# Optimization experiments

Measured on AMD Instinct MI355X. Metric: run time of the kernel, lower is better.

Reference implementation:

```python
import jax, jax.numpy as jnp
import numpy as np

K = 7          # kernel_size (square)
P = K // 2     # padding
NUM_HEADS = 12


def setup_inputs() -> dict:
    key = jax.random.key(0)
    ks = jax.random.split(key, 6)
    B, H, W, D = 16, 56, 56, 768
    x = jax.random.normal(ks[0], (B, H, W, D), jnp.float32)
    qkv_w = jax.random.normal(ks[1], (3 * D, D), jnp.float32) * 0.02
    qkv_b = jnp.zeros((3 * D,), jnp.float32)
    rel_bias = jax.random.normal(ks[2], (1, NUM_HEADS, 1, K * K), jnp.float32)
    proj_w = jax.random.normal(ks[3], (D, D), jnp.float32) * 0.02
    proj_b = jnp.zeros((D,), jnp.float32)
    return {"x": x, "qkv_w": qkv_w, "qkv_b": qkv_b, "rel_bias": rel_bias,
            "proj_w": proj_w, "proj_b": proj_b}


def reference(x, qkv_w, qkv_b, rel_bias, proj_w, proj_b):
    B, H, W, D = x.shape
    hd = D // NUM_HEADS
    scale = 1.0 / np.sqrt(hd)

    qkv = x @ qkv_w.T + qkv_b                       # [B,H,W,3D]
    qkv = jnp.pad(qkv, ((0, 0), (P, P), (P, P), (0, 0)))  # zero-pad spatially
    Hp, Wp = H + 2 * P, W + 2 * P
    qkv = qkv.reshape(B, Hp, Wp, 3, NUM_HEADS, hd)
    qkv = jnp.transpose(qkv, (3, 0, 4, 1, 2, 5))    # [3,B,nh,Hp,Wp,hd]
    qf, kf, vf = qkv[0], qkv[1], qkv[2]

    q = qf[:, :, P:P + H, P:P + W, :]               # [B,nh,H,W,hd] (center pixel queries)

    # validity of each padded position (out-of-bounds keys get -inf, matching the torch mask)
    valid = jnp.pad(jnp.ones((H, W), dtype=bool), ((P, P), (P, P)))

    # scores per kernel offset; offsets iterate row-major (di, dj) matching
    # torch.meshgrid(..., indexing='ij') flattening used for relative_position_bias
    scores = []
    for di in range(K):
        for dj in range(K):
            ksh = kf[:, :, di:di + H, dj:dj + W, :]           # shifted keys [B,nh,H,W,hd]
            s = jnp.einsum('bnhwd,bnhwd->bnhw', q, ksh) * scale
            s = s + rel_bias[0, :, 0, di * K + dj][None, :, None, None]
            vmask = valid[di:di + H, dj:dj + W]
            s = jnp.where(vmask[None, None, :, :], s, -jnp.inf)
            scores.append(s)
    scores = jnp.stack(scores, axis=-1)             # [B,nh,H,W,K*K]
    attn = jax.nn.softmax(scores, axis=-1)

    out = jnp.zeros_like(q)
    for di in range(K):
        for dj in range(K):
            vsh = vf[:, :, di:di + H, dj:dj + W, :]
            out = out + attn[..., di * K + dj, None] * vsh

    out = jnp.transpose(out, (0, 2, 3, 1, 4)).reshape(B, H, W, D)
    return out @ proj_w.T + proj_b
```

## Files before the change

kernel.cpp:

```cpp
#include <hip/hip_runtime.h>
#include <hip/hip_bf16.h>

typedef __attribute__((ext_vector_type(8))) short short8;
typedef __attribute__((ext_vector_type(4))) short s16x4;
typedef __attribute__((ext_vector_type(4))) float f32x4;

#define AS1 __attribute__((address_space(1)))
#define AS3 __attribute__((address_space(3)))

__device__ __forceinline__ void gld16(const short* g, short* l) {
  __builtin_amdgcn_global_load_lds((const AS1 void*)g, (AS3 void*)l, 16, 0, 0);
}

__device__ __forceinline__ float bf2f(short x) {
  return __uint_as_float(((unsigned)(unsigned short)x) << 16);
}
__device__ __forceinline__ short f2bf(float f) {
  unsigned u = __float_as_uint(f);
  return (short)((u + 0x7fffu + ((u >> 16) & 1u)) >> 16);
}

__global__ void cast_f32_bf16(const float* __restrict__ src, short* __restrict__ dst, int n8) {
  int stride = gridDim.x * blockDim.x;
  for (int i = blockIdx.x * blockDim.x + threadIdx.x; i < n8; i += stride) {
    const float4* s = (const float4*)(src + (size_t)i * 8);
    float4 a = s[0], b = s[1];
    short8 o;
    o[0] = f2bf(a.x); o[1] = f2bf(a.y); o[2] = f2bf(a.z); o[3] = f2bf(a.w);
    o[4] = f2bf(b.x); o[5] = f2bf(b.y); o[6] = f2bf(b.z); o[7] = f2bf(b.w);
    *(short8*)(dst + (size_t)i * 8) = o;
  }
}

template<int OUT_BF16>
__global__ __launch_bounds__(256, 2) void gemm_bt(
    const short* __restrict__ A, const short* __restrict__ Bm,
    const float* __restrict__ bias, void* __restrict__ C,
    int M, int N, int Kd, int NB)
{
  __shared__ short As[128 * 64];
  __shared__ short Bs[128 * 64];
  const int tid = threadIdx.x;
  const int wave = tid >> 6, lane = tid & 63;

  int nwg = gridDim.x;
  int chunk = nwg >> 3;
  int bid = blockIdx.x;
  int nb2 = (bid & 7) * chunk + (bid >> 3);
  int per = NB << 3;
  int sr = nb2 / per, rem = nb2 - sr * per;
  int nblk = rem >> 3, mrow = rem & 7;
  int mblk = sr * 8 + mrow;

  size_t arow0 = (size_t)mblk * 128;
  size_t brow0 = (size_t)nblk * 128;
  const int wm = wave >> 1, wn = wave & 1;
  const int lr = lane & 15, grp = lane >> 4;

  const short* gsa[4]; const short* gsb[4];
  short* lda[4]; short* ldb[4];
  #pragma unroll
  for (int i = 0; i < 4; ++i) {
    int f = i * 256 + wave * 64 + lane;
    int row = f >> 3;
    int colc = (f & 7) ^ (row & 7);
    gsa[i] = A  + (arow0 + row) * Kd + colc * 8;
    gsb[i] = Bm + (brow0 + row) * Kd + colc * 8;
    lda[i] = &As[(i * 256 + wave * 64) * 8];
    ldb[i] = &Bs[(i * 256 + wave * 64) * 8];
  }

  f32x4 acc[4][4];
  #pragma unroll
  for (int i = 0; i < 4; ++i)
    #pragma unroll
    for (int j = 0; j < 4; ++j) {
      acc[i][j][0] = 0.f; acc[i][j][1] = 0.f; acc[i][j][2] = 0.f; acc[i][j][3] = 0.f;
    }

  int aoff[4][2], boff[4][2];
  #pragma unroll
  for (int mi = 0; mi < 4; ++mi) {
    int arow = wm * 64 + mi * 16 + lr;
    int brow = wn * 64 + mi * 16 + lr;
    #pragma unroll
    for (int kk = 0; kk < 2; ++kk) {
      int cb = (kk * 64 + grp * 16);
      aoff[mi][kk] = arow * 64 + ((cb ^ ((arow & 7) << 4)) >> 1);
      boff[mi][kk] = brow * 64 + ((cb ^ ((brow & 7) << 4)) >> 1);
    }
  }

  for (int k0 = 0; k0 < Kd; k0 += 64) {
    #pragma unroll
    for (int i = 0; i < 4; ++i) {
      gld16(gsa[i] + k0, lda[i]);
      gld16(gsb[i] + k0, ldb[i]);
    }
    __syncthreads();
    short8 af[4][2], bfr[4][2];
    #pragma unroll
    for (int mi = 0; mi < 4; ++mi)
      #pragma unroll
      for (int kk = 0; kk < 2; ++kk) {
        af[mi][kk]  = *(const short8*)&As[aoff[mi][kk]];
        bfr[mi][kk] = *(const short8*)&Bs[boff[mi][kk]];
      }
    #pragma unroll
    for (int kk = 0; kk < 2; ++kk)
      #pragma unroll
      for (int i = 0; i < 4; ++i)
        #pragma unroll
        for (int j = 0; j < 4; ++j)
          acc[i][j] = __builtin_amdgcn_mfma_f32_16x16x32_bf16(af[i][kk], bfr[j][kk], acc[i][j], 0, 0, 0);
    __syncthreads();
  }

  int r0 = grp * 4;
  #pragma unroll
  for (int i = 0; i < 4; ++i) {
    size_t grow0 = arow0 + wm * 64 + i * 16 + r0;
    #pragma unroll
    for (int j = 0; j < 4; ++j) {
      size_t gcol = brow0 + wn * 64 + j * 16 + lr;
      float bv = bias[gcol];
      #pragma unroll
      for (int r = 0; r < 4; ++r) {
        float v = acc[i][j][r] + bv;
        size_t off = (grow0 + r) * (size_t)N + gcol;
        if (OUT_BF16) ((short*)C)[off] = f2bf(v);
        else          ((float*)C)[off] = v;
      }
    }
  }
}

#define HALO_V 232
#define PROW 168

__global__ __launch_bounds__(256, 3) void attn_mfma(
    const short* __restrict__ qkv, const float* __restrict__ rel_bias,
    short* __restrict__ attn_out)
{
  __shared__ __align__(16) short kvbuf[HALO_V * 64];
  __shared__ __align__(16) short pbuf[4 * 16 * PROW];
  __shared__ float sbias[49];

  const int tid = threadIdx.x;
  const int wave = tid >> 6, lane = tid & 63;
  const int ht = blockIdx.x >> 2, wt = blockIdx.x & 3;
  const int head = blockIdx.y % 12, b = blockIdx.y / 12;
  const int r0 = ht * 4, c0 = wt * 16;
  const int grp = lane >> 4;
  const int q   = lane & 15;
  const int grp4 = grp * 4, grp8 = grp * 8;
  const int Sw = (22 * wave) & ~7;

  if (tid < 49) sbias[tid] = rel_bias[head * 49 + tid];

  #pragma unroll
  for (int it = 0; it < 8; ++it) {
    int idx = it * 256 + tid;
    if (idx < HALO_V * 8) {
      int vec = idx >> 3, c = idx & 7;
      int hr = vec / 22, hc = vec - hr * 22;
      int gh = r0 - 3 + hr, gw = c0 - 3 + hc;
      short8 val = {};
      if (vec < 220 && (unsigned)gh < 56u && (unsigned)gw < 56u)
        val = *(const short8*)(qkv + ((size_t)((b * 56 + gh) * 56 + gw)) * 2304
                               + 768 + head * 64 + c * 8);
      *(short8*)&kvbuf[vec * 64 + ((c ^ (vec & 7))) * 8] = val;
    }
  }

  const int qrow = r0 + wave;
  const int qcol = min(c0 + q, 55);
  const short* qp = qkv + ((size_t)((b * 56 + qrow) * 56 + qcol)) * 2304 + head * 64;
  short8 qf0 = *(const short8*)(qp + grp8);
  short8 qf1 = *(const short8*)(qp + 32 + grp8);

  __syncthreads();

  f32x4 accs[10];
  #pragma unroll
  for (int kt = 0; kt < 10; ++kt) {
    accs[kt][0] = 0.f; accs[kt][1] = 0.f; accs[kt][2] = 0.f; accs[kt][3] = 0.f;
  }
  #pragma unroll
  for (int kt = 0; kt < 10; ++kt) {
    int vec = Sw + kt * 16 + q;
    int sw = vec & 7;
    short8 k0 = *(const short8*)&kvbuf[vec * 64 + ((grp ^ sw)) * 8];
    short8 k1 = *(const short8*)&kvbuf[vec * 64 + (((grp + 4) ^ sw)) * 8];
    accs[kt] = __builtin_amdgcn_mfma_f32_16x16x32_bf16(k0, qf0, accs[kt], 0, 0, 0);
    accs[kt] = __builtin_amdgcn_mfma_f32_16x16x32_bf16(k1, qf1, accs[kt], 0, 0, 0);
  }

  __syncthreads();

  if (tid < HALO_V) {
    int vec = tid;
    int hr = vec / 22, hc = vec - hr * 22;
    int gh = r0 - 3 + hr, gw = c0 - 3 + hc;
    bool v = (vec < 220) && ((unsigned)gh < 56u) && ((unsigned)gw < 56u);
    int ghc = v ? gh : 0, gwc = v ? gw : 0;
    const short* vp = qkv + ((size_t)((b * 56 + ghc) * 56 + gwc)) * 2304
                      + 1536 + head * 64;
    #pragma unroll
    for (int c = 0; c < 8; ++c) {
      short8 val = {};
      if (v) val = *(const short8*)(vp + c * 8);
      #pragma unroll
      for (int j = 0; j < 8; ++j)
        kvbuf[(c * 8 + j) * HALO_V + vec] = val[j];
    }
  }

  float sv[10][4];
  float mx = -1e30f;
  #pragma unroll
  for (int kt = 0; kt < 10; ++kt) {
    #pragma unroll
    for (int r = 0; r < 4; ++r) {
      int i22 = Sw + kt * 16 + grp4 + r;
      int hr = i22 / 22, hc = i22 - hr * 22;
      int dr = hr - wave, dc = hc - q;
      int kh = r0 - 3 + hr, kw = c0 - 3 + hc;
      bool valid = ((unsigned)dr < 7u) && ((unsigned)dc < 7u) &&
                   ((unsigned)kh < 56u) && ((unsigned)kw < 56u);
      int o = valid ? (dr * 7 + dc) : 0;
      float s = accs[kt][r] * 0.125f + sbias[o];
      s = valid ? s : -1e30f;
      sv[kt][r] = s;
      mx = fmaxf(mx, s);
    }
  }
  mx = fmaxf(mx, __shfl_xor(mx, 16));
  mx = fmaxf(mx, __shfl_xor(mx, 32));
  float sum = 0.f;
  #pragma unroll
  for (int kt = 0; kt < 10; ++kt)
    #pragma unroll
    for (int r = 0; r < 4; ++r) {
      float e = __expf(sv[kt][r] - mx);
      sv[kt][r] = e;
      sum += e;
    }
  sum += __shfl_xor(sum, 16);
  sum += __shfl_xor(sum, 32);
  float inv = 1.0f / sum;

  short* pb = pbuf + wave * 16 * PROW;
  #pragma unroll
  for (int kt = 0; kt < 10; ++kt) {
    s16x4 pk;
    #pragma unroll
    for (int r = 0; r < 4; ++r) pk[r] = f2bf(sv[kt][r] * inv);
    *(s16x4*)&pb[q * PROW + kt * 16 + grp4] = pk;
  }

  __syncthreads();

  f32x4 acco[4];
  #pragma unroll
  for (int dt = 0; dt < 4; ++dt) {
    acco[dt][0] = 0.f; acco[dt][1] = 0.f; acco[dt][2] = 0.f; acco[dt][3] = 0.f;
  }
  #pragma unroll
  for (int km = 0; km < 5; ++km) {
    short8 pf = *(const short8*)&pb[q * PROW + km * 32 + grp8];
    #pragma unroll
    for (int dt = 0; dt < 4; ++dt) {
      short8 vf = *(const short8*)&kvbuf[(dt * 16 + q) * HALO_V + Sw + km * 32 + grp8];
      acco[dt] = __builtin_amdgcn_mfma_f32_16x16x32_bf16(pf, vf, acco[dt], 0, 0, 0);
    }
  }

  #pragma unroll
  for (int dt = 0; dt < 4; ++dt) {
    #pragma unroll
    for (int r = 0; r < 4; ++r) {
      int qc = c0 + grp4 + r;
      if (qc < 56) {
        size_t off = ((size_t)((b * 56 + qrow) * 56 + qc)) * 768
                     + head * 64 + dt * 16 + q;
        attn_out[off] = f2bf(acco[dt][r]);
      }
    }
  }
}

extern "C" void kernel_launch(void* const* d_in, const int* in_sizes, int n_in,
                              void* d_out, int out_size, void* d_ws, size_t ws_size,
                              hipStream_t stream)
{
  const float* x      = (const float*)d_in[0];
  const float* qkv_w  = (const float*)d_in[1];
  const float* qkv_b  = (const float*)d_in[2];
  const float* rel_b  = (const float*)d_in[3];
  const float* proj_w = (const float*)d_in[4];
  const float* proj_b = (const float*)d_in[5];

  char* ws = (char*)d_ws;
  short* x_bf    = (short*)(ws);
  short* attn_bf = (short*)(ws);
  short* qw_bf   = (short*)(ws + 77070336);
  short* pw_bf   = (short*)(ws + 80609280);
  short* qkv_bf  = (short*)(ws + 81788928);

  cast_f32_bf16<<<2048, 256, 0, stream>>>(x, x_bf, 38535168 / 8);
  cast_f32_bf16<<<864, 256, 0, stream>>>(qkv_w, qw_bf, 1769472 / 8);
  cast_f32_bf16<<<288, 256, 0, stream>>>(proj_w, pw_bf, 589824 / 8);

  gemm_bt<1><<<392 * 18, 256, 0, stream>>>(x_bf, qw_bf, qkv_b, (void*)qkv_bf,
                                           50176, 2304, 768, 18);

  attn_mfma<<<dim3(56, 192), 256, 0, stream>>>(qkv_bf, rel_b, attn_bf);

  gemm_bt<0><<<392 * 6, 256, 0, stream>>>(attn_bf, pw_bf, proj_b, d_out,
                                          50176, 768, 768, 6);
}
```

Baseline: 530.1 us.

## Async K halo loads, prefetch V into registers, precompute bias indices, defer normalization

The K halo is now loaded straight into LDS with global_load_lds, with a zero buffer standing in for padded positions. V rows are prefetched into registers before the QK MFMAs and transposed into LDS after the softmax, so their global latency overlaps compute. Per-lane bias and validity indices come from a small table built by a separate kernel, replacing the per-element divide and mask arithmetic. Softmax normalization moves to the output stage, using the hardware bf16 conversion. The cost is more registers and a table read per lane, which may hurt occupancy.

```diff
diff --git a/kernel.cpp b/kernel.cpp
--- a/kernel.cpp
+++ b/kernel.cpp
@@ -18,6 +18,10 @@
 __device__ __forceinline__ short f2bf(float f) {
   unsigned u = __float_as_uint(f);
   return (short)((u + 0x7fffu + ((u >> 16) & 1u)) >> 16);
+}
+__device__ __forceinline__ short f2bfn(float f) {
+  __hip_bfloat16 h = __float2bfloat16(f);
+  return *reinterpret_cast<short*>(&h);
 }
 
 __global__ void cast_f32_bf16(const float* __restrict__ src, short* __restrict__ dst, int n8) {
@@ -135,43 +139,66 @@
   }
 }
 
+__global__ void build_idx(unsigned char* __restrict__ idxt) {
+  int tile = blockIdx.x;
+  int ht = tile >> 2, wt = tile & 3;
+  int tid = threadIdx.x;
+  int wave = tid >> 6, lane = tid & 63;
+  int grp = lane >> 4, q = lane & 15;
+  int Sw = (22 * wave) & ~7;
+  unsigned w[12];
+  #pragma unroll
+  for (int i = 0; i < 12; ++i) w[i] = 0x31313131u;
+  #pragma unroll
+  for (int kt = 0; kt < 10; ++kt) {
+    unsigned wd = 0;
+    #pragma unroll
+    for (int r = 0; r < 4; ++r) {
+      int i22 = Sw + kt * 16 + grp * 4 + r;
+      int hr = i22 / 22, hc = i22 - hr * 22;
+      int dr = hr - wave, dc = hc - q;
+      int kh = ht * 4 - 3 + hr, kw = wt * 16 - 3 + hc;
+      bool valid = ((unsigned)dr < 7u) && ((unsigned)dc < 7u) &&
+                   ((unsigned)kh < 56u) && ((unsigned)kw < 56u);
+      unsigned o = valid ? (unsigned)(dr * 7 + dc) : 49u;
+      wd |= o << (r * 8);
+    }
+    w[kt] = wd;
+  }
+  uint4* dst = (uint4*)(idxt + (((size_t)tile * 4 + wave) * 64 + lane) * 48);
+  dst[0] = make_uint4(w[0], w[1], w[2], w[3]);
+  dst[1] = make_uint4(w[4], w[5], w[6], w[7]);
+  dst[2] = make_uint4(w[8], w[9], w[10], w[11]);
+}
+
 #define HALO_V 232
 #define PROW 168
 
 __global__ __launch_bounds__(256, 3) void attn_mfma(
     const short* __restrict__ qkv, const float* __restrict__ rel_bias,
+    const unsigned char* __restrict__ idxt, const short* __restrict__ zp,
     short* __restrict__ attn_out)
 {
   __shared__ __align__(16) short kvbuf[HALO_V * 64];
   __shared__ __align__(16) short pbuf[4 * 16 * PROW];
-  __shared__ float sbias[49];
+  __shared__ float sbias[52];
 
   const int tid = threadIdx.x;
   const int wave = tid >> 6, lane = tid & 63;
-  const int ht = blockIdx.x >> 2, wt = blockIdx.x & 3;
+  const int tile = blockIdx.x;
+  const int ht = tile >> 2, wt = tile & 3;
   const int head = blockIdx.y % 12, b = blockIdx.y / 12;
   const int r0 = ht * 4, c0 = wt * 16;
-  const int grp = lane >> 4;
-  const int q   = lane & 15;
+  const int grp = lane >> 4, q = lane & 15;
   const int grp4 = grp * 4, grp8 = grp * 8;
   const int Sw = (22 * wave) & ~7;
 
-  if (tid < 49) sbias[tid] = rel_bias[head * 49 + tid];
-
-  #pragma unroll
-  for (int it = 0; it < 8; ++it) {
-    int idx = it * 256 + tid;
-    if (idx < HALO_V * 8) {
-      int vec = idx >> 3, c = idx & 7;
-      int hr = vec / 22, hc = vec - hr * 22;
-      int gh = r0 - 3 + hr, gw = c0 - 3 + hc;
-      short8 val = {};
-      if (vec < 220 && (unsigned)gh < 56u && (unsigned)gw < 56u)
-        val = *(const short8*)(qkv + ((size_t)((b * 56 + gh) * 56 + gw)) * 2304
-                               + 768 + head * 64 + c * 8);
-      *(short8*)&kvbuf[vec * 64 + ((c ^ (vec & 7))) * 8] = val;
-    }
-  }
+  if (tid < 50) sbias[tid] = (tid < 49) ? rel_bias[head * 49 + tid] : -1e30f;
+
+  const uint4* ip = (const uint4*)(idxt + (((size_t)tile * 4 + wave) * 64 + lane) * 48);
+  uint4 iw0 = ip[0], iw1 = ip[1], iw2 = ip[2];
+  unsigned idxw[10] = {iw0.x, iw0.y, iw0.z, iw0.w, iw1.x, iw1.y, iw1.z, iw1.w,
+                       iw2.x, iw2.y};
 
   const int qrow = r0 + wave;
   const int qcol = min(c0 + q, 55);
@@ -179,7 +206,42 @@
   short8 qf0 = *(const short8*)(qp + grp8);
   short8 qf1 = *(const short8*)(qp + 32 + grp8);
 
+  #pragma unroll
+  for (int it = 0; it < 8; ++it) {
+    int f = it * 256 + tid;
+    if (f < HALO_V * 8) {
+      int row = f >> 3, cc = f & 7;
+      int hr = row / 22, hc = row - hr * 22;
+      int gh = r0 - 3 + hr, gw = c0 - 3 + hc;
+      bool ok = (row < 220) && ((unsigned)gh < 56u) && ((unsigned)gw < 56u);
+      const short* src = ok
+        ? qkv + ((size_t)((b * 56 + gh) * 56 + gw)) * 2304 + 768 + head * 64
+              + ((cc ^ (row & 7)) * 8)
+        : zp;
+      gld16(src, &kvbuf[(it * 256 + wave * 64) * 8]);
+    }
+  }
+
   __syncthreads();
+
+  short8 va[4], vb[4];
+  int vq = 0, dcc = 0;
+  const bool vact = (tid < HALO_V);
+  if (vact) {
+    vq = tid % 58; dcc = tid / 58;
+    #pragma unroll
+    for (int rr = 0; rr < 4; ++rr) {
+      int vec = vq * 4 + rr;
+      int hr = vec / 22, hc = vec - hr * 22;
+      int gh = r0 - 3 + hr, gw = c0 - 3 + hc;
+      bool ok = (vec < 220) && ((unsigned)gh < 56u) && ((unsigned)gw < 56u);
+      const short8* vp = ok
+        ? (const short8*)(qkv + ((size_t)((b * 56 + gh) * 56 + gw)) * 2304
+                          + 1536 + head * 64 + dcc * 16)
+        : (const short8*)zp;
+      va[rr] = vp[0]; vb[rr] = vp[1];
+    }
+  }
 
   f32x4 accs[10];
   #pragma unroll
@@ -198,40 +260,14 @@
 
   __syncthreads();
 
-  if (tid < HALO_V) {
-    int vec = tid;
-    int hr = vec / 22, hc = vec - hr * 22;
-    int gh = r0 - 3 + hr, gw = c0 - 3 + hc;
-    bool v = (vec < 220) && ((unsigned)gh < 56u) && ((unsigned)gw < 56u);
-    int ghc = v ? gh : 0, gwc = v ? gw : 0;
-    const short* vp = qkv + ((size_t)((b * 56 + ghc) * 56 + gwc)) * 2304
-                      + 1536 + head * 64;
-    #pragma unroll
-    for (int c = 0; c < 8; ++c) {
-      short8 val = {};
-      if (v) val = *(const short8*)(vp + c * 8);
-      #pragma unroll
-      for (int j = 0; j < 8; ++j)
-        kvbuf[(c * 8 + j) * HALO_V + vec] = val[j];
-    }
-  }
-
-  float sv[10][4];
   float mx = -1e30f;
   #pragma unroll
   for (int kt = 0; kt < 10; ++kt) {
     #pragma unroll
     for (int r = 0; r < 4; ++r) {
-      int i22 = Sw + kt * 16 + grp4 + r;
-      int hr = i22 / 22, hc = i22 - hr * 22;
-      int dr = hr - wave, dc = hc - q;
-      int kh = r0 - 3 + hr, kw = c0 - 3 + hc;
-      bool valid = ((unsigned)dr < 7u) && ((unsigned)dc < 7u) &&
-                   ((unsigned)kh < 56u) && ((unsigned)kw < 56u);
-      int o = valid ? (dr * 7 + dc) : 0;
-      float s = accs[kt][r] * 0.125f + sbias[o];
-      s = valid ? s : -1e30f;
-      sv[kt][r] = s;
+      float bia = sbias[(idxw[kt] >> (r * 8)) & 0xffu];
+      float s = fmaf(accs[kt][r], 0.125f, bia);
+      accs[kt][r] = s;
       mx = fmaxf(mx, s);
     }
   }
@@ -242,20 +278,35 @@
   for (int kt = 0; kt < 10; ++kt)
     #pragma unroll
     for (int r = 0; r < 4; ++r) {
-      float e = __expf(sv[kt][r] - mx);
-      sv[kt][r] = e;
+      float e = __expf(accs[kt][r] - mx);
+      accs[kt][r] = e;
       sum += e;
     }
   sum += __shfl_xor(sum, 16);
   sum += __shfl_xor(sum, 32);
   float inv = 1.0f / sum;
 
+  if (vact) {
+    #pragma unroll
+    for (int dd = 0; dd < 8; ++dd) {
+      s16x4 w;
+      w[0] = va[0][dd]; w[1] = va[1][dd]; w[2] = va[2][dd]; w[3] = va[3][dd];
+      *(s16x4*)&kvbuf[(dcc * 16 + dd) * HALO_V + vq * 4] = w;
+    }
+    #pragma unroll
+    for (int dd = 0; dd < 8; ++dd) {
+      s16x4 w;
+      w[0] = vb[0][dd]; w[1] = vb[1][dd]; w[2] = vb[2][dd]; w[3] = vb[3][dd];
+      *(s16x4*)&kvbuf[(dcc * 16 + 8 + dd) * HALO_V + vq * 4] = w;
+    }
+  }
+
   short* pb = pbuf + wave * 16 * PROW;
   #pragma unroll
   for (int kt = 0; kt < 10; ++kt) {
     s16x4 pk;
     #pragma unroll
-    for (int r = 0; r < 4; ++r) pk[r] = f2bf(sv[kt][r] * inv);
+    for (int r = 0; r < 4; ++r) pk[r] = f2bfn(accs[kt][r]);
     *(s16x4*)&pb[q * PROW + kt * 16 + grp4] = pk;
   }
 
@@ -276,6 +327,9 @@
     }
   }
 
+  float invr[4];
+  #pragma unroll
+  for (int r = 0; r < 4; ++r) invr[r] = __shfl(inv, grp4 + r);
   #pragma unroll
   for (int dt = 0; dt < 4; ++dt) {
     #pragma unroll
@@ -284,7 +338,7 @@
       if (qc < 56) {
         size_t off = ((size_t)((b * 56 + qrow) * 56 + qc)) * 768
                      + head * 64 + dt * 16 + q;
-        attn_out[off] = f2bf(acco[dt][r]);
+        attn_out[off] = f2bfn(acco[dt][r] * invr[r]);
       }
     }
   }
@@ -307,6 +361,11 @@
   short* qw_bf   = (short*)(ws + 77070336);
   short* pw_bf   = (short*)(ws + 80609280);
   short* qkv_bf  = (short*)(ws + 81788928);
+  unsigned char* idxt = (unsigned char*)(ws + 312999936);
+  short* zp      = (short*)(ws + 313688064);
+
+  hipMemsetAsync(zp, 0, 256, stream);
+  build_idx<<<56, 256, 0, stream>>>(idxt);
 
   cast_f32_bf16<<<2048, 256, 0, stream>>>(x, x_bf, 38535168 / 8);
   cast_f32_bf16<<<864, 256, 0, stream>>>(qkv_w, qw_bf, 1769472 / 8);
@@ -315,7 +374,7 @@
   gemm_bt<1><<<392 * 18, 256, 0, stream>>>(x_bf, qw_bf, qkv_b, (void*)qkv_bf,
                                            50176, 2304, 768, 18);
 
-  attn_mfma<<<dim3(56, 192), 256, 0, stream>>>(qkv_bf, rel_b, attn_bf);
+  attn_mfma<<<dim3(56, 192), 256, 0, stream>>>(qkv_bf, rel_b, idxt, zp, attn_bf);
 
   gemm_bt<0><<<392 * 6, 256, 0, stream>>>(attn_bf, pw_bf, proj_b, d_out,
                                           50176, 768, 768, 6);
```

After: 457.9 us. -13.6%, faster.
